# Kernel tuning notes

Measured on AMD Instinct MI355X. Metric: run time of the kernel, lower is better.

Reference implementation:

```python
import jax, jax.numpy as jnp
import numpy as np

B, H, L, DK = 1, 16, 2048, 64
F_FACTOR = 64            # f
MAX_SEQ = 2048           # max_seq_len
RB = MAX_SEQ // F_FACTOR # 32, out dim of f_b


def setup_inputs() -> dict:
    key = jax.random.key(0)
    ks = jax.random.split(key, 6)
    q = jax.random.normal(ks[0], (B, H, L, DK), dtype=jnp.float32)
    v = jax.random.normal(ks[1], (B, H, L, DK), dtype=jnp.float32)
    # nn.Linear weights: [out_features, in_features]
    Wa = jax.random.normal(ks[2], (F_FACTOR, DK), dtype=jnp.float32) / np.sqrt(DK)
    ba = jax.random.normal(ks[3], (F_FACTOR,), dtype=jnp.float32) * 0.02
    Wb = jax.random.normal(ks[4], (RB, DK), dtype=jnp.float32) / np.sqrt(DK)
    bb = jax.random.normal(ks[5], (RB,), dtype=jnp.float32) * 0.02
    return {"q": q, "v": v, "Wa": Wa, "ba": ba, "Wb": Wb, "bb": bb, "len_q": L}


def reference(q, v, Wa, ba, Wb, bb, len_q):
    f = Wa.shape[0]            # f
    rb = Wb.shape[0]           # max_seq_len // f
    # h_a: repeat each of the f factor channels (max_seq_len//f) times -> [B,H,L,max_seq_len], slice to len_q
    h_a = jnp.repeat(q @ Wa.T + ba, rb, axis=-1)[..., :len_q]
    # h_b: repeat each of the (max_seq_len//f) channels f times
    h_b = jnp.repeat(q @ Wb.T + bb, f, axis=-1)[..., :len_q]
    # dense_attn = h_a @ h_b^T  -> [B,H,L,L]
    dense_attn = jnp.einsum('bhik,bhjk->bhij', h_a, h_b)
    # mask=None path; dropout inactive (eval / p=0)
    dense_attn = jax.nn.softmax(dense_attn, axis=-1)
    output = jnp.matmul(dense_attn, v)  # [B,H,L,DK]
    return (output, dense_attn)
```

## Files before the change

kernel.cpp:

```cpp
#include <hip/hip_runtime.h>
#include <hip/hip_bf16.h>


#define HN 16
#define LN 2048
#define KR 32

typedef __attribute__((ext_vector_type(8))) short bf16x8;
typedef __attribute__((ext_vector_type(4))) float f32x4;

__device__ __forceinline__ float b2f(unsigned short u) {
    return __uint_as_float(((unsigned int)u) << 16);
}
__device__ __forceinline__ unsigned short f2b(float f) {
    __hip_bfloat16 h = __float2bfloat16(f);
    return *reinterpret_cast<unsigned short*>(&h);
}

__global__ __launch_bounds__(256) void k_cb(
    const float* __restrict__ q,
    const float* __restrict__ Wa, const float* __restrict__ ba,
    const float* __restrict__ Wb, const float* __restrict__ bb,
    unsigned short* __restrict__ Chi, unsigned short* __restrict__ Clo,
    unsigned short* __restrict__ Bhi, unsigned short* __restrict__ Blo)
{
    __shared__ float sWa[64 * 64];
    __shared__ float sWb[32 * 64];
    __shared__ float sba[64];
    __shared__ float sbb[32];
    const int tid = threadIdx.x;
    for (int i = tid; i < 64 * 64; i += 256) sWa[i] = Wa[i];
    for (int i = tid; i < 32 * 64; i += 256) sWb[i] = Wb[i];
    if (tid < 64) sba[tid] = ba[tid];
    if (tid < 32) sbb[tid] = bb[tid];
    __syncthreads();

    const int t = blockIdx.x * 256 + tid;
    const int row = t >> 1, mh = (t & 1) * 16;
    float qf[64];
    const float4* q4p = reinterpret_cast<const float4*>(q + (size_t)row * 64);
    #pragma unroll
    for (int k4 = 0; k4 < 16; ++k4) {
        float4 u = q4p[k4];
        qf[4*k4+0] = u.x; qf[4*k4+1] = u.y; qf[4*k4+2] = u.z; qf[4*k4+3] = u.w;
    }
    const int ob = row * KR;
    #pragma unroll 1
    for (int mi = 0; mi < 16; ++mi) {
        const int m = mh + mi;
        float a0 = sba[2*m], a1 = sba[2*m+1], bv = sbb[m];
        const float4* wa0 = reinterpret_cast<const float4*>(&sWa[(2*m) * 64]);
        const float4* wa1 = reinterpret_cast<const float4*>(&sWa[(2*m+1) * 64]);
        const float4* wb0 = reinterpret_cast<const float4*>(&sWb[m * 64]);
        #pragma unroll
        for (int k4 = 0; k4 < 16; ++k4) {
            float4 w0 = wa0[k4], w1 = wa1[k4], w2 = wb0[k4];
            float x0 = qf[4*k4], x1 = qf[4*k4+1], x2 = qf[4*k4+2], x3 = qf[4*k4+3];
            a0 = fmaf(x0, w0.x, a0); a0 = fmaf(x1, w0.y, a0);
            a0 = fmaf(x2, w0.z, a0); a0 = fmaf(x3, w0.w, a0);
            a1 = fmaf(x0, w1.x, a1); a1 = fmaf(x1, w1.y, a1);
            a1 = fmaf(x2, w1.z, a1); a1 = fmaf(x3, w1.w, a1);
            bv = fmaf(x0, w2.x, bv); bv = fmaf(x1, w2.y, bv);
            bv = fmaf(x2, w2.z, bv); bv = fmaf(x3, w2.w, bv);
        }
        float c = 32.f * (a0 + a1);
        unsigned short ch = f2b(c);
        Chi[ob + m] = ch; Clo[ob + m] = f2b(c - b2f(ch));
        unsigned short bh = f2b(bv);
        Bhi[ob + m] = bh; Blo[ob + m] = f2b(bv - b2f(bh));
    }
}

__global__ __launch_bounds__(256) void k_vt(
    const float* __restrict__ v, unsigned short* __restrict__ Vt)
{
    __shared__ unsigned short sv[64 * 66];
    const int tid = threadIdx.x;
    const int h = blockIdx.x >> 5, jt = blockIdx.x & 31;
    const float* src = v + (size_t)(h * LN + jt * 64) * 64;
    for (int i = tid; i < 4096; i += 256)
        sv[(i >> 6) * 66 + (i & 63)] = f2b(src[i]);
    __syncthreads();
    for (int i = tid; i < 4096; i += 256) {
        int d = i >> 6, j = i & 63;
        Vt[(size_t)(h * 64 + d) * LN + jt * 64 + j] = sv[j * 66 + d];
    }
}

__global__ __launch_bounds__(256) void k_stats(
    const unsigned short* __restrict__ Chi, const unsigned short* __restrict__ Clo,
    const unsigned short* __restrict__ Bhi, const unsigned short* __restrict__ Blo,
    float* __restrict__ rowM, float* __restrict__ rowLinv)
{
    const int h = blockIdx.x >> 5, tile = blockIdx.x & 31;
    const int tid = threadIdx.x, w = tid >> 6, lane = tid & 63;
    const int quad = lane >> 4, n16 = lane & 15;
    const int rbase = tile * 64 + w * 16;
    const int hL = h * LN;

    const bf16x8 ahi = *reinterpret_cast<const bf16x8*>(Chi + (size_t)(hL + rbase + n16) * KR + quad * 8);
    const bf16x8 alo = *reinterpret_cast<const bf16x8*>(Clo + (size_t)(hL + rbase + n16) * KR + quad * 8);

    const unsigned short* bhiP = Bhi + (size_t)(hL + n16) * KR + quad * 8;
    const unsigned short* bloP = Blo + (size_t)(hL + n16) * KR + quad * 8;

    float m0[4] = {-1e30f, -1e30f, -1e30f, -1e30f};
    float l0[4] = {0.f, 0.f, 0.f, 0.f};

    for (int jc = 0; jc < 32; ++jc) {
        const int jb = jc * 64;
        f32x4 s[4];
        #pragma unroll
        for (int ni = 0; ni < 4; ++ni) {
            const int off = (jb + ni * 16) * KR;
            bf16x8 bhi = *reinterpret_cast<const bf16x8*>(bhiP + off);
            bf16x8 blo = *reinterpret_cast<const bf16x8*>(bloP + off);
            f32x4 acc = {0.f, 0.f, 0.f, 0.f};
            acc = __builtin_amdgcn_mfma_f32_16x16x32_bf16(ahi, bhi, acc, 0, 0, 0);
            acc = __builtin_amdgcn_mfma_f32_16x16x32_bf16(ahi, blo, acc, 0, 0, 0);
            acc = __builtin_amdgcn_mfma_f32_16x16x32_bf16(alo, bhi, acc, 0, 0, 0);
            acc = __builtin_amdgcn_mfma_f32_16x16x32_bf16(alo, blo, acc, 0, 0, 0);
            s[ni] = acc;
        }
        #pragma unroll
        for (int r = 0; r < 4; ++r) {
            float v0 = s[0][r], v1 = s[1][r], v2 = s[2][r], v3 = s[3][r];
            float mx = fmaxf(fmaxf(v0, v1), fmaxf(v2, v3));
            float mn = fmaxf(m0[r], mx);
            l0[r] = l0[r] * __expf(m0[r] - mn)
                  + __expf(v0 - mn) + __expf(v1 - mn)
                  + __expf(v2 - mn) + __expf(v3 - mn);
            m0[r] = mn;
        }
    }
    #pragma unroll
    for (int off = 1; off <= 8; off <<= 1) {
        #pragma unroll
        for (int r = 0; r < 4; ++r) {
            float m2 = __shfl_xor(m0[r], off, 64);
            float l2 = __shfl_xor(l0[r], off, 64);
            float mn = fmaxf(m0[r], m2);
            l0[r] = l0[r] * __expf(m0[r] - mn) + l2 * __expf(m2 - mn);
            m0[r] = mn;
        }
    }
    if (n16 == 0) {
        #pragma unroll
        for (int r = 0; r < 4; ++r) {
            const int grow = rbase + quad * 4 + r;
            rowM[hL + grow] = m0[r];
            rowLinv[hL + grow] = 1.f / l0[r];
        }
    }
}

__global__ __launch_bounds__(256) void k_pv(
    const unsigned short* __restrict__ Chi, const unsigned short* __restrict__ Clo,
    const unsigned short* __restrict__ Bhi, const unsigned short* __restrict__ Blo,
    const unsigned short* __restrict__ Vt,
    const float* __restrict__ rowM, const float* __restrict__ rowLinv,
    float* __restrict__ outO, float* __restrict__ outP)
{
    __shared__ unsigned short Ps[4][16 * 68];
    const int h = blockIdx.x >> 5, tile = blockIdx.x & 31;
    const int tid = threadIdx.x, w = tid >> 6, lane = tid & 63;
    const int quad = lane >> 4, n16 = lane & 15;
    const int rbase = tile * 64 + w * 16;
    const int hL = h * LN;
    unsigned short* ps = &Ps[w][0];

    const bf16x8 ahi = *reinterpret_cast<const bf16x8*>(Chi + (size_t)(hL + rbase + n16) * KR + quad * 8);
    const bf16x8 alo = *reinterpret_cast<const bf16x8*>(Clo + (size_t)(hL + rbase + n16) * KR + quad * 8);

    const unsigned short* bhiP = Bhi + (size_t)(hL + n16) * KR + quad * 8;
    const unsigned short* bloP = Blo + (size_t)(hL + n16) * KR + quad * 8;

    const unsigned short* vrow[4];
    #pragma unroll
    for (int di = 0; di < 4; ++di)
        vrow[di] = Vt + (size_t)(h * 64 + di * 16 + n16) * LN + quad * 8;

    float mr[4], li[4];
    float* pP[4];
    #pragma unroll
    for (int r = 0; r < 4; ++r) {
        mr[r] = rowM[hL + rbase + quad * 4 + r];
        li[r] = rowLinv[hL + rbase + quad * 4 + r];
        pP[r] = outP + (size_t)(hL + rbase + quad * 4 + r) * LN + n16;
    }
    f32x4 zero = {0.f, 0.f, 0.f, 0.f};
    f32x4 o[4];
    #pragma unroll
    for (int di = 0; di < 4; ++di) o[di] = zero;

    for (int jc = 0; jc < 32; ++jc) {
        const int jb = jc * 64;
        #pragma unroll
        for (int ni = 0; ni < 4; ++ni) {
            const int off = (jb + ni * 16) * KR;
            bf16x8 bhi = *reinterpret_cast<const bf16x8*>(bhiP + off);
            bf16x8 blo = *reinterpret_cast<const bf16x8*>(bloP + off);
            f32x4 acc = zero;
            acc = __builtin_amdgcn_mfma_f32_16x16x32_bf16(ahi, bhi, acc, 0, 0, 0);
            acc = __builtin_amdgcn_mfma_f32_16x16x32_bf16(ahi, blo, acc, 0, 0, 0);
            acc = __builtin_amdgcn_mfma_f32_16x16x32_bf16(alo, bhi, acc, 0, 0, 0);
            acc = __builtin_amdgcn_mfma_f32_16x16x32_bf16(alo, blo, acc, 0, 0, 0);
            #pragma unroll
            for (int r = 0; r < 4; ++r) {
                float p = __expf(acc[r] - mr[r]) * li[r];
                pP[r][jb + ni * 16] = p;
                ps[(quad * 4 + r) * 68 + ni * 16 + n16] = f2b(p);
            }
        }
        #pragma unroll
        for (int ks = 0; ks < 2; ++ks) {
            const bf16x8 pa = *reinterpret_cast<const bf16x8*>(ps + n16 * 68 + ks * 32 + quad * 8);
            #pragma unroll
            for (int di = 0; di < 4; ++di) {
                const bf16x8 vb = *reinterpret_cast<const bf16x8*>(vrow[di] + jb + ks * 32);
                o[di] = __builtin_amdgcn_mfma_f32_16x16x32_bf16(pa, vb, o[di], 0, 0, 0);
            }
        }
    }
    #pragma unroll
    for (int di = 0; di < 4; ++di) {
        #pragma unroll
        for (int r = 0; r < 4; ++r) {
            const int grow = rbase + quad * 4 + r;
            outO[(size_t)(hL + grow) * 64 + di * 16 + n16] = o[di][r];
        }
    }
}

extern "C" void kernel_launch(void* const* d_in, const int* in_sizes, int n_in,
                              void* d_out, int out_size, void* d_ws, size_t ws_size,
                              hipStream_t stream)
{
    (void)in_sizes; (void)n_in; (void)out_size; (void)ws_size;
    const float* q  = (const float*)d_in[0];
    const float* v  = (const float*)d_in[1];
    const float* Wa = (const float*)d_in[2];
    const float* ba = (const float*)d_in[3];
    const float* Wb = (const float*)d_in[4];
    const float* bb = (const float*)d_in[5];

    float* out = (float*)d_out;
    char* wsb = (char*)d_ws;
    const size_t CBb = (size_t)HN * LN * KR * 2;
    unsigned short* Chi = (unsigned short*)(wsb + 0 * CBb);
    unsigned short* Clo = (unsigned short*)(wsb + 1 * CBb);
    unsigned short* Bhi = (unsigned short*)(wsb + 2 * CBb);
    unsigned short* Blo = (unsigned short*)(wsb + 3 * CBb);
    unsigned short* Vt  = (unsigned short*)(wsb + 4 * CBb);
    float* rowM    = (float*)(wsb + 6 * CBb);
    float* rowLinv = (float*)(wsb + 6 * CBb + (size_t)HN * LN * 4);

    float* outO = out;
    float* outP = out + (size_t)HN * LN * 64;

    hipLaunchKernelGGL(k_cb, dim3(256), dim3(256), 0, stream,
                       q, Wa, ba, Wb, bb, Chi, Clo, Bhi, Blo);
    hipLaunchKernelGGL(k_vt, dim3(512), dim3(256), 0, stream, v, Vt);
    hipLaunchKernelGGL(k_stats, dim3(512), dim3(256), 0, stream,
                       Chi, Clo, Bhi, Blo, rowM, rowLinv);
    hipLaunchKernelGGL(k_pv, dim3(512), dim3(256), 0, stream,
                       Chi, Clo, Bhi, Blo, Vt, rowM, rowLinv, outO, outP);
}
```

Measured before the change: 443.2 us.

## Fuse softmax stats and PV passes into one kernel with vectorized P stores

Merges the row-statistics kernel and the probability/PV kernel into a single kernel that computes max and sum in a first sweep and then recomputes scores, writing P and accumulating O. This removes one launch and the rowM/rowLinv round trip through global memory. P tiles are staged in fp32 shared memory so each wave can write them as coalesced 16-byte nontemporal stores instead of scattered scalar stores. The change also remaps block indices to interleave heads and doubles the k_cb grid so each thread computes fewer output channels. In exchange it uses more shared memory per block, which may lower occupancy.

```diff
diff --git a/kernel.cpp b/kernel.cpp
--- a/kernel.cpp
+++ b/kernel.cpp
@@ -36,7 +36,7 @@
     __syncthreads();
 
     const int t = blockIdx.x * 256 + tid;
-    const int row = t >> 1, mh = (t & 1) * 16;
+    const int row = t >> 2, mh = (t & 3) * 8;
     float qf[64];
     const float4* q4p = reinterpret_cast<const float4*>(q + (size_t)row * 64);
     #pragma unroll
@@ -46,7 +46,7 @@
     }
     const int ob = row * KR;
     #pragma unroll 1
-    for (int mi = 0; mi < 16; ++mi) {
+    for (int mi = 0; mi < 8; ++mi) {
         const int m = mh + mi;
         float a0 = sba[2*m], a1 = sba[2*m+1], bv = sbb[m];
         const float4* wa0 = reinterpret_cast<const float4*>(&sWa[(2*m) * 64]);
@@ -87,16 +87,23 @@
     }
 }
 
-__global__ __launch_bounds__(256) void k_stats(
+__global__ __launch_bounds__(256) void k_pvs(
     const unsigned short* __restrict__ Chi, const unsigned short* __restrict__ Clo,
     const unsigned short* __restrict__ Bhi, const unsigned short* __restrict__ Blo,
-    float* __restrict__ rowM, float* __restrict__ rowLinv)
-{
-    const int h = blockIdx.x >> 5, tile = blockIdx.x & 31;
+    const unsigned short* __restrict__ Vt,
+    float* __restrict__ outO, float* __restrict__ outP)
+{
+    __shared__ unsigned short Ps[4][16 * 68];
+    __shared__ float Psf[4][16 * 68];
+    const int b = blockIdx.x;
+    const int h = (b & 7) * 2 + (b >> 8);
+    const int tile = (b >> 3) & 31;
     const int tid = threadIdx.x, w = tid >> 6, lane = tid & 63;
     const int quad = lane >> 4, n16 = lane & 15;
     const int rbase = tile * 64 + w * 16;
     const int hL = h * LN;
+    unsigned short* ps = &Ps[w][0];
+    float* psf = &Psf[w][0];
 
     const bf16x8 ahi = *reinterpret_cast<const bf16x8*>(Chi + (size_t)(hL + rbase + n16) * KR + quad * 8);
     const bf16x8 alo = *reinterpret_cast<const bf16x8*>(Clo + (size_t)(hL + rbase + n16) * KR + quad * 8);
@@ -104,9 +111,15 @@
     const unsigned short* bhiP = Bhi + (size_t)(hL + n16) * KR + quad * 8;
     const unsigned short* bloP = Blo + (size_t)(hL + n16) * KR + quad * 8;
 
+    const unsigned short* vrow[4];
+    #pragma unroll
+    for (int di = 0; di < 4; ++di)
+        vrow[di] = Vt + (size_t)(h * 64 + di * 16 + n16) * LN + quad * 8;
+
+    f32x4 zero = {0.f, 0.f, 0.f, 0.f};
+
     float m0[4] = {-1e30f, -1e30f, -1e30f, -1e30f};
     float l0[4] = {0.f, 0.f, 0.f, 0.f};
-
     for (int jc = 0; jc < 32; ++jc) {
         const int jb = jc * 64;
         f32x4 s[4];
@@ -115,7 +128,7 @@
             const int off = (jb + ni * 16) * KR;
             bf16x8 bhi = *reinterpret_cast<const bf16x8*>(bhiP + off);
             bf16x8 blo = *reinterpret_cast<const bf16x8*>(bloP + off);
-            f32x4 acc = {0.f, 0.f, 0.f, 0.f};
+            f32x4 acc = zero;
             acc = __builtin_amdgcn_mfma_f32_16x16x32_bf16(ahi, bhi, acc, 0, 0, 0);
             acc = __builtin_amdgcn_mfma_f32_16x16x32_bf16(ahi, blo, acc, 0, 0, 0);
             acc = __builtin_amdgcn_mfma_f32_16x16x32_bf16(alo, bhi, acc, 0, 0, 0);
@@ -144,51 +157,10 @@
             m0[r] = mn;
         }
     }
-    if (n16 == 0) {
-        #pragma unroll
-        for (int r = 0; r < 4; ++r) {
-            const int grow = rbase + quad * 4 + r;
-            rowM[hL + grow] = m0[r];
-            rowLinv[hL + grow] = 1.f / l0[r];
-        }
-    }
-}
-
-__global__ __launch_bounds__(256) void k_pv(
-    const unsigned short* __restrict__ Chi, const unsigned short* __restrict__ Clo,
-    const unsigned short* __restrict__ Bhi, const unsigned short* __restrict__ Blo,
-    const unsigned short* __restrict__ Vt,
-    const float* __restrict__ rowM, const float* __restrict__ rowLinv,
-    float* __restrict__ outO, float* __restrict__ outP)
-{
-    __shared__ unsigned short Ps[4][16 * 68];
-    const int h = blockIdx.x >> 5, tile = blockIdx.x & 31;
-    const int tid = threadIdx.x, w = tid >> 6, lane = tid & 63;
-    const int quad = lane >> 4, n16 = lane & 15;
-    const int rbase = tile * 64 + w * 16;
-    const int hL = h * LN;
-    unsigned short* ps = &Ps[w][0];
-
-    const bf16x8 ahi = *reinterpret_cast<const bf16x8*>(Chi + (size_t)(hL + rbase + n16) * KR + quad * 8);
-    const bf16x8 alo = *reinterpret_cast<const bf16x8*>(Clo + (size_t)(hL + rbase + n16) * KR + quad * 8);
-
-    const unsigned short* bhiP = Bhi + (size_t)(hL + n16) * KR + quad * 8;
-    const unsigned short* bloP = Blo + (size_t)(hL + n16) * KR + quad * 8;
-
-    const unsigned short* vrow[4];
-    #pragma unroll
-    for (int di = 0; di < 4; ++di)
-        vrow[di] = Vt + (size_t)(h * 64 + di * 16 + n16) * LN + quad * 8;
-
     float mr[4], li[4];
-    float* pP[4];
-    #pragma unroll
-    for (int r = 0; r < 4; ++r) {
-        mr[r] = rowM[hL + rbase + quad * 4 + r];
-        li[r] = rowLinv[hL + rbase + quad * 4 + r];
-        pP[r] = outP + (size_t)(hL + rbase + quad * 4 + r) * LN + n16;
-    }
-    f32x4 zero = {0.f, 0.f, 0.f, 0.f};
+    #pragma unroll
+    for (int r = 0; r < 4; ++r) { mr[r] = m0[r]; li[r] = 1.f / l0[r]; }
+
     f32x4 o[4];
     #pragma unroll
     for (int di = 0; di < 4; ++di) o[di] = zero;
@@ -208,9 +180,18 @@
             #pragma unroll
             for (int r = 0; r < 4; ++r) {
                 float p = __expf(acc[r] - mr[r]) * li[r];
-                pP[r][jb + ni * 16] = p;
-                ps[(quad * 4 + r) * 68 + ni * 16 + n16] = f2b(p);
+                const int sidx = (quad * 4 + r) * 68 + ni * 16 + n16;
+                psf[sidx] = p;
+                ps[sidx] = f2b(p);
             }
+        }
+        #pragma unroll
+        for (int rr = 0; rr < 4; ++rr) {
+            const int prow = rr * 4 + quad;
+            const int pcol = n16 * 4;
+            f32x4 val = *reinterpret_cast<f32x4*>(psf + prow * 68 + pcol);
+            __builtin_nontemporal_store(val,
+                reinterpret_cast<f32x4*>(outP + (size_t)(hL + rbase + prow) * LN + jb + pcol));
         }
         #pragma unroll
         for (int ks = 0; ks < 2; ++ks) {
@@ -227,7 +208,8 @@
         #pragma unroll
         for (int r = 0; r < 4; ++r) {
             const int grow = rbase + quad * 4 + r;
-            outO[(size_t)(hL + grow) * 64 + di * 16 + n16] = o[di][r];
+            __builtin_nontemporal_store(o[di][r],
+                &outO[(size_t)(hL + grow) * 64 + di * 16 + n16]);
         }
     }
 }
@@ -252,17 +234,13 @@
     unsigned short* Bhi = (unsigned short*)(wsb + 2 * CBb);
     unsigned short* Blo = (unsigned short*)(wsb + 3 * CBb);
     unsigned short* Vt  = (unsigned short*)(wsb + 4 * CBb);
-    float* rowM    = (float*)(wsb + 6 * CBb);
-    float* rowLinv = (float*)(wsb + 6 * CBb + (size_t)HN * LN * 4);
 
     float* outO = out;
     float* outP = out + (size_t)HN * LN * 64;
 
-    hipLaunchKernelGGL(k_cb, dim3(256), dim3(256), 0, stream,
+    hipLaunchKernelGGL(k_cb, dim3(512), dim3(256), 0, stream,
                        q, Wa, ba, Wb, bb, Chi, Clo, Bhi, Blo);
     hipLaunchKernelGGL(k_vt, dim3(512), dim3(256), 0, stream, v, Vt);
-    hipLaunchKernelGGL(k_stats, dim3(512), dim3(256), 0, stream,
-                       Chi, Clo, Bhi, Blo, rowM, rowLinv);
-    hipLaunchKernelGGL(k_pv, dim3(512), dim3(256), 0, stream,
-                       Chi, Clo, Bhi, Blo, Vt, rowM, rowLinv, outO, outP);
-}
+    hipLaunchKernelGGL(k_pvs, dim3(512), dim3(256), 0, stream,
+                       Chi, Clo, Bhi, Blo, Vt, outO, outP);
+}
```

Result: no change. 449.6 us (+1.5%).

## Split key range across blocks, stage B tiles in LDS via async loads

Applied to the files above, without the earlier changes.

Key dimension is split: the stats kernel runs 4 partial key ranges per row tile and writes partial max/sum, merged in the PV kernel. The PV kernel splits keys in two and writes partial outputs, which a new reduction kernel adds. B operands are stored in a tiled, MFMA-fragment-friendly layout and double-buffered into LDS with global_load_lds. Output stores become nontemporal and k_cb writes vectorized. This raises parallelism from 512 blocks and reduces per-lane scattered global loads, at the cost of an extra kernel, extra partial-output traffic and more LDS per block.

```diff
diff --git a/kernel.cpp b/kernel.cpp
--- a/kernel.cpp
+++ b/kernel.cpp
@@ -16,13 +16,20 @@
     __hip_bfloat16 h = __float2bfloat16(f);
     return *reinterpret_cast<unsigned short*>(&h);
 }
+__device__ __forceinline__ void glds16(const void* g, void* l) {
+    __builtin_amdgcn_global_load_lds(
+        (const __attribute__((address_space(1))) unsigned int*)g,
+        (__attribute__((address_space(3))) unsigned int*)l, 16, 0, 0);
+}
+
+#define TILE_B 4096
 
 __global__ __launch_bounds__(256) void k_cb(
     const float* __restrict__ q,
     const float* __restrict__ Wa, const float* __restrict__ ba,
     const float* __restrict__ Wb, const float* __restrict__ bb,
     unsigned short* __restrict__ Chi, unsigned short* __restrict__ Clo,
-    unsigned short* __restrict__ Bhi, unsigned short* __restrict__ Blo)
+    unsigned short* __restrict__ TileB)
 {
     __shared__ float sWa[64 * 64];
     __shared__ float sWb[32 * 64];
@@ -36,7 +43,10 @@
     __syncthreads();
 
     const int t = blockIdx.x * 256 + tid;
-    const int row = t >> 1, mh = (t & 1) * 16;
+    const int row = t >> 2, kg = t & 3, mh = kg * 8;
+    const int h = row >> 11, i = row & 2047;
+    const int jc = i >> 6, c = i & 63;
+
     float qf[64];
     const float4* q4p = reinterpret_cast<const float4*>(q + (size_t)row * 64);
     #pragma unroll
@@ -44,9 +54,9 @@
         float4 u = q4p[k4];
         qf[4*k4+0] = u.x; qf[4*k4+1] = u.y; qf[4*k4+2] = u.z; qf[4*k4+3] = u.w;
     }
-    const int ob = row * KR;
-    #pragma unroll 1
-    for (int mi = 0; mi < 16; ++mi) {
+    unsigned short chb[8], clb[8], bhb[8], blb[8];
+    #pragma unroll
+    for (int mi = 0; mi < 8; ++mi) {
         const int m = mh + mi;
         float a0 = sba[2*m], a1 = sba[2*m+1], bv = sbb[m];
         const float4* wa0 = reinterpret_cast<const float4*>(&sWa[(2*m) * 64]);
@@ -63,12 +73,17 @@
             bv = fmaf(x0, w2.x, bv); bv = fmaf(x1, w2.y, bv);
             bv = fmaf(x2, w2.z, bv); bv = fmaf(x3, w2.w, bv);
         }
-        float c = 32.f * (a0 + a1);
-        unsigned short ch = f2b(c);
-        Chi[ob + m] = ch; Clo[ob + m] = f2b(c - b2f(ch));
+        float cc = 32.f * (a0 + a1);
+        unsigned short ch = f2b(cc);
+        chb[mi] = ch; clb[mi] = f2b(cc - b2f(ch));
         unsigned short bh = f2b(bv);
-        Bhi[ob + m] = bh; Blo[ob + m] = f2b(bv - b2f(bh));
-    }
+        bhb[mi] = bh; blb[mi] = f2b(bv - b2f(bh));
+    }
+    *reinterpret_cast<uint4*>(Chi + (size_t)row * KR + mh) = *reinterpret_cast<uint4*>(chb);
+    *reinterpret_cast<uint4*>(Clo + (size_t)row * KR + mh) = *reinterpret_cast<uint4*>(clb);
+    unsigned short* tb = TileB + (size_t)(h * 32 + jc) * TILE_B + (kg * 64 + c) * 8;
+    *reinterpret_cast<uint4*>(tb)        = *reinterpret_cast<uint4*>(bhb);
+    *reinterpret_cast<uint4*>(tb + 2048) = *reinterpret_cast<uint4*>(blb);
 }
 
 __global__ __launch_bounds__(256) void k_vt(
@@ -89,10 +104,14 @@
 
 __global__ __launch_bounds__(256) void k_stats(
     const unsigned short* __restrict__ Chi, const unsigned short* __restrict__ Clo,
-    const unsigned short* __restrict__ Bhi, const unsigned short* __restrict__ Blo,
-    float* __restrict__ rowM, float* __restrict__ rowLinv)
-{
-    const int h = blockIdx.x >> 5, tile = blockIdx.x & 31;
+    const unsigned short* __restrict__ TileB,
+    float* __restrict__ rowM4, float* __restrict__ rowL4)
+{
+    __shared__ unsigned short sB[2][TILE_B];
+    const int b = blockIdx.x;
+    const int h = (b & 7) * 2 + (b >> 10);
+    const int tile = (b >> 3) & 31;
+    const int j4 = (b >> 8) & 3;
     const int tid = threadIdx.x, w = tid >> 6, lane = tid & 63;
     const int quad = lane >> 4, n16 = lane & 15;
     const int rbase = tile * 64 + w * 16;
@@ -101,21 +120,37 @@
     const bf16x8 ahi = *reinterpret_cast<const bf16x8*>(Chi + (size_t)(hL + rbase + n16) * KR + quad * 8);
     const bf16x8 alo = *reinterpret_cast<const bf16x8*>(Clo + (size_t)(hL + rbase + n16) * KR + quad * 8);
 
-    const unsigned short* bhiP = Bhi + (size_t)(hL + n16) * KR + quad * 8;
-    const unsigned short* bloP = Blo + (size_t)(hL + n16) * KR + quad * 8;
-
+    const char* tBase = (const char*)(TileB + (size_t)(h * 32) * TILE_B);
+    const int fragB = (quad * 64 + n16) * 8;
+    const int srcOff = w * 2048 + lane * 16;
+    const int jc0 = j4 * 8;
+
+    f32x4 zero = {0.f, 0.f, 0.f, 0.f};
     float m0[4] = {-1e30f, -1e30f, -1e30f, -1e30f};
     float l0[4] = {0.f, 0.f, 0.f, 0.f};
 
-    for (int jc = 0; jc < 32; ++jc) {
-        const int jb = jc * 64;
+    {
+        const char* g = tBase + (size_t)jc0 * 8192;
+        char* d = (char*)sB[0];
+        glds16(g + srcOff, d + w * 2048);
+        glds16(g + srcOff + 1024, d + w * 2048 + 1024);
+    }
+    for (int ji = 0; ji < 8; ++ji) {
+        __syncthreads();
+        const int cur = ji & 1;
+        if (ji + 1 < 8) {
+            const char* g = tBase + (size_t)(jc0 + ji + 1) * 8192;
+            char* d = (char*)sB[cur ^ 1];
+            glds16(g + srcOff, d + w * 2048);
+            glds16(g + srcOff + 1024, d + w * 2048 + 1024);
+        }
+        const unsigned short* t = sB[cur];
         f32x4 s[4];
         #pragma unroll
         for (int ni = 0; ni < 4; ++ni) {
-            const int off = (jb + ni * 16) * KR;
-            bf16x8 bhi = *reinterpret_cast<const bf16x8*>(bhiP + off);
-            bf16x8 blo = *reinterpret_cast<const bf16x8*>(bloP + off);
-            f32x4 acc = {0.f, 0.f, 0.f, 0.f};
+            bf16x8 bhi = *reinterpret_cast<const bf16x8*>(t + fragB + ni * 128);
+            bf16x8 blo = *reinterpret_cast<const bf16x8*>(t + 2048 + fragB + ni * 128);
+            f32x4 acc = zero;
             acc = __builtin_amdgcn_mfma_f32_16x16x32_bf16(ahi, bhi, acc, 0, 0, 0);
             acc = __builtin_amdgcn_mfma_f32_16x16x32_bf16(ahi, blo, acc, 0, 0, 0);
             acc = __builtin_amdgcn_mfma_f32_16x16x32_bf16(alo, bhi, acc, 0, 0, 0);
@@ -147,22 +182,25 @@
     if (n16 == 0) {
         #pragma unroll
         for (int r = 0; r < 4; ++r) {
-            const int grow = rbase + quad * 4 + r;
-            rowM[hL + grow] = m0[r];
-            rowLinv[hL + grow] = 1.f / l0[r];
-        }
-    }
-}
-
-__global__ __launch_bounds__(256) void k_pv(
+            const size_t idx = (size_t)(hL + rbase + quad * 4 + r) * 4 + j4;
+            rowM4[idx] = m0[r];
+            rowL4[idx] = l0[r];
+        }
+    }
+}
+
+__global__ __launch_bounds__(256, 4) void k_pv(
     const unsigned short* __restrict__ Chi, const unsigned short* __restrict__ Clo,
-    const unsigned short* __restrict__ Bhi, const unsigned short* __restrict__ Blo,
-    const unsigned short* __restrict__ Vt,
-    const float* __restrict__ rowM, const float* __restrict__ rowLinv,
-    float* __restrict__ outO, float* __restrict__ outP)
-{
+    const unsigned short* __restrict__ TileB, const unsigned short* __restrict__ Vt,
+    const float* __restrict__ rowM4, const float* __restrict__ rowL4,
+    float* __restrict__ oPart, float* __restrict__ outP)
+{
+    __shared__ unsigned short sB[2][TILE_B];
     __shared__ unsigned short Ps[4][16 * 68];
-    const int h = blockIdx.x >> 5, tile = blockIdx.x & 31;
+    const int b = blockIdx.x;
+    const int h = (b & 7) * 2 + (b >> 9);
+    const int tile = (b >> 3) & 31;
+    const int jh = (b >> 8) & 1;
     const int tid = threadIdx.x, w = tid >> 6, lane = tid & 63;
     const int quad = lane >> 4, n16 = lane & 15;
     const int rbase = tile * 64 + w * 16;
@@ -172,8 +210,10 @@
     const bf16x8 ahi = *reinterpret_cast<const bf16x8*>(Chi + (size_t)(hL + rbase + n16) * KR + quad * 8);
     const bf16x8 alo = *reinterpret_cast<const bf16x8*>(Clo + (size_t)(hL + rbase + n16) * KR + quad * 8);
 
-    const unsigned short* bhiP = Bhi + (size_t)(hL + n16) * KR + quad * 8;
-    const unsigned short* bloP = Blo + (size_t)(hL + n16) * KR + quad * 8;
+    const char* tBase = (const char*)(TileB + (size_t)(h * 32) * TILE_B);
+    const int fragB = (quad * 64 + n16) * 8;
+    const int srcOff = w * 2048 + lane * 16;
+    const int jc0 = jh * 16;
 
     const unsigned short* vrow[4];
     #pragma unroll
@@ -181,25 +221,44 @@
         vrow[di] = Vt + (size_t)(h * 64 + di * 16 + n16) * LN + quad * 8;
 
     float mr[4], li[4];
-    float* pP[4];
     #pragma unroll
     for (int r = 0; r < 4; ++r) {
-        mr[r] = rowM[hL + rbase + quad * 4 + r];
-        li[r] = rowLinv[hL + rbase + quad * 4 + r];
-        pP[r] = outP + (size_t)(hL + rbase + quad * 4 + r) * LN + n16;
-    }
+        const size_t idx = (size_t)(hL + rbase + quad * 4 + r) * 4;
+        float ma = rowM4[idx], mb = rowM4[idx+1], mc = rowM4[idx+2], md = rowM4[idx+3];
+        float la = rowL4[idx], lb = rowL4[idx+1], lc = rowL4[idx+2], ld = rowL4[idx+3];
+        float m = fmaxf(fmaxf(ma, mb), fmaxf(mc, md));
+        float l = la * __expf(ma - m) + lb * __expf(mb - m)
+                + lc * __expf(mc - m) + ld * __expf(md - m);
+        mr[r] = m;
+        li[r] = 1.f / l;
+    }
+
     f32x4 zero = {0.f, 0.f, 0.f, 0.f};
     f32x4 o[4];
     #pragma unroll
     for (int di = 0; di < 4; ++di) o[di] = zero;
 
-    for (int jc = 0; jc < 32; ++jc) {
-        const int jb = jc * 64;
+    {
+        const char* g = tBase + (size_t)jc0 * 8192;
+        char* d = (char*)sB[0];
+        glds16(g + srcOff, d + w * 2048);
+        glds16(g + srcOff + 1024, d + w * 2048 + 1024);
+    }
+    for (int ji = 0; ji < 16; ++ji) {
+        __syncthreads();
+        const int cur = ji & 1;
+        if (ji + 1 < 16) {
+            const char* g = tBase + (size_t)(jc0 + ji + 1) * 8192;
+            char* d = (char*)sB[cur ^ 1];
+            glds16(g + srcOff, d + w * 2048);
+            glds16(g + srcOff + 1024, d + w * 2048 + 1024);
+        }
+        const unsigned short* t = sB[cur];
+        const int jb = (jc0 + ji) * 64;
         #pragma unroll
         for (int ni = 0; ni < 4; ++ni) {
-            const int off = (jb + ni * 16) * KR;
-            bf16x8 bhi = *reinterpret_cast<const bf16x8*>(bhiP + off);
-            bf16x8 blo = *reinterpret_cast<const bf16x8*>(bloP + off);
+            bf16x8 bhi = *reinterpret_cast<const bf16x8*>(t + fragB + ni * 128);
+            bf16x8 blo = *reinterpret_cast<const bf16x8*>(t + 2048 + fragB + ni * 128);
             f32x4 acc = zero;
             acc = __builtin_amdgcn_mfma_f32_16x16x32_bf16(ahi, bhi, acc, 0, 0, 0);
             acc = __builtin_amdgcn_mfma_f32_16x16x32_bf16(ahi, blo, acc, 0, 0, 0);
@@ -208,7 +267,8 @@
             #pragma unroll
             for (int r = 0; r < 4; ++r) {
                 float p = __expf(acc[r] - mr[r]) * li[r];
-                pP[r][jb + ni * 16] = p;
+                __builtin_nontemporal_store(p,
+                    outP + (size_t)(hL + rbase + quad * 4 + r) * LN + jb + ni * 16 + n16);
                 ps[(quad * 4 + r) * 68 + ni * 16 + n16] = f2b(p);
             }
         }
@@ -222,14 +282,26 @@
             }
         }
     }
+    float* op = oPart + (size_t)jh * HN * LN * 64;
     #pragma unroll
     for (int di = 0; di < 4; ++di) {
         #pragma unroll
         for (int r = 0; r < 4; ++r) {
             const int grow = rbase + quad * 4 + r;
-            outO[(size_t)(hL + grow) * 64 + di * 16 + n16] = o[di][r];
-        }
-    }
+            op[(size_t)(hL + grow) * 64 + di * 16 + n16] = o[di][r];
+        }
+    }
+}
+
+__global__ __launch_bounds__(256) void k_ored(
+    const float* __restrict__ oPart, float* __restrict__ outO)
+{
+    const int i = blockIdx.x * 256 + threadIdx.x;
+    const f32x4* p0 = reinterpret_cast<const f32x4*>(oPart);
+    const f32x4* p1 = reinterpret_cast<const f32x4*>(oPart + (size_t)HN * LN * 64);
+    f32x4 a = p0[i], b = p1[i];
+    f32x4 s = {a[0] + b[0], a[1] + b[1], a[2] + b[2], a[3] + b[3]};
+    __builtin_nontemporal_store(s, reinterpret_cast<f32x4*>(outO) + i);
 }
 
 extern "C" void kernel_launch(void* const* d_in, const int* in_sizes, int n_in,
@@ -246,23 +318,24 @@
 
     float* out = (float*)d_out;
     char* wsb = (char*)d_ws;
-    const size_t CBb = (size_t)HN * LN * KR * 2;
-    unsigned short* Chi = (unsigned short*)(wsb + 0 * CBb);
-    unsigned short* Clo = (unsigned short*)(wsb + 1 * CBb);
-    unsigned short* Bhi = (unsigned short*)(wsb + 2 * CBb);
-    unsigned short* Blo = (unsigned short*)(wsb + 3 * CBb);
-    unsigned short* Vt  = (unsigned short*)(wsb + 4 * CBb);
-    float* rowM    = (float*)(wsb + 6 * CBb);
-    float* rowLinv = (float*)(wsb + 6 * CBb + (size_t)HN * LN * 4);
+    const size_t MB = 1024 * 1024;
+    unsigned short* Chi   = (unsigned short*)(wsb);
+    unsigned short* Clo   = (unsigned short*)(wsb + 2 * MB);
+    unsigned short* TileB = (unsigned short*)(wsb + 4 * MB);
+    unsigned short* Vt    = (unsigned short*)(wsb + 8 * MB);
+    float* rowM4 = (float*)(wsb + 12 * MB);
+    float* rowL4 = (float*)(wsb + 12 * MB + 512 * 1024);
+    float* oPart = (float*)(wsb + 13 * MB);
 
     float* outO = out;
     float* outP = out + (size_t)HN * LN * 64;
 
-    hipLaunchKernelGGL(k_cb, dim3(256), dim3(256), 0, stream,
-                       q, Wa, ba, Wb, bb, Chi, Clo, Bhi, Blo);
+    hipLaunchKernelGGL(k_cb, dim3(512), dim3(256), 0, stream,
+                       q, Wa, ba, Wb, bb, Chi, Clo, TileB);
     hipLaunchKernelGGL(k_vt, dim3(512), dim3(256), 0, stream, v, Vt);
-    hipLaunchKernelGGL(k_stats, dim3(512), dim3(256), 0, stream,
-                       Chi, Clo, Bhi, Blo, rowM, rowLinv);
-    hipLaunchKernelGGL(k_pv, dim3(512), dim3(256), 0, stream,
-                       Chi, Clo, Bhi, Blo, Vt, rowM, rowLinv, outO, outP);
-}
+    hipLaunchKernelGGL(k_stats, dim3(2048), dim3(256), 0, stream,
+                       Chi, Clo, TileB, rowM4, rowL4);
+    hipLaunchKernelGGL(k_pv, dim3(1024), dim3(256), 0, stream,
+                       Chi, Clo, TileB, Vt, rowM4, rowL4, oPart, outP);
+    hipLaunchKernelGGL(k_ored, dim3(2048), dim3(256), 0, stream, oPart, outO);
+}
```

New measurement: 420.9 us. -5.0%, faster.
